# Optimization experiments

Measured on AMD Instinct MI355X. Metric: run time of the kernel, lower is better.

## Reference

```python
import jax, jax.numpy as jnp
import numpy as np

B = 64            # graphs in batch
N = 100_000       # total nodes
E = 600_000       # total edges of g == nodes of line graph lg
E2 = 1_500_000    # edges of line graph
H = 128           # hidden_dim
L = 3             # num_layers
MAXZ = 100

seg_sum = jax.ops.segment_sum


def setup_inputs() -> dict:
    key = jax.random.key(0)
    ks = jax.random.split(key, 20)
    s = 1.0 / np.sqrt(H)
    inp = {
        'z': jax.random.randint(ks[0], (N,), 0, MAXZ + 1),
        'd': jax.random.uniform(ks[1], (E, 1), dtype=jnp.float32),
        'src': jax.random.randint(ks[2], (E,), 0, N),
        'dst': jax.random.randint(ks[3], (E,), 0, N),
        'lsrc': jax.random.randint(ks[4], (E2,), 0, E),
        'ldst': jax.random.randint(ks[5], (E2,), 0, E),
        'node_graph': jnp.sort(jax.random.randint(ks[6], (N,), 0, B)),
        'edge_graph': jnp.sort(jax.random.randint(ks[7], (E,), 0, B)),
        'emb': jax.random.normal(ks[8], (MAXZ + 1, H), jnp.float32),
        'ep_w': jax.random.normal(ks[9], (1, H), jnp.float32) * s,
        'ep_b': jnp.zeros((H,), jnp.float32),
        'gW': jax.random.normal(ks[10], (L, H, H), jnp.float32) * s,
        'gb': jnp.zeros((L, H), jnp.float32),
        'lgW': jax.random.normal(ks[11], (L, H, H), jnp.float32) * s,
        'lgb': jnp.zeros((L, H), jnp.float32),
        'r1w': jax.random.normal(ks[12], (2 * H, H), jnp.float32) * s,
        'r1b': jnp.zeros((H,), jnp.float32),
        'r2w': jax.random.normal(ks[13], (H, 1), jnp.float32) * s,
        'r2b': jnp.zeros((1,), jnp.float32),
    }
    return inp


def _graph_conv(h, srcix, dstix, W, b, n_nodes):
    # DGL GraphConv, norm='both', aggregate-then-weight (in==out dims):
    # h' = D_in^{-1/2} * A^T * (D_out^{-1/2} * h) @ W + b, degrees clamped >= 1
    ones = jnp.ones(srcix.shape[0], h.dtype)
    deg_out = jnp.clip(seg_sum(ones, srcix, num_segments=n_nodes), 1.0)
    deg_in = jnp.clip(seg_sum(ones, dstix, num_segments=n_nodes), 1.0)
    m = h * (deg_out ** -0.5)[:, None]
    agg = seg_sum(m[srcix], dstix, num_segments=n_nodes)  # SpMM gather-scatter
    agg = agg * (deg_in ** -0.5)[:, None]
    return agg @ W + b


def _segment_mean(h, seg, n_seg):
    sums = seg_sum(h, seg, num_segments=n_seg)
    cnt = jnp.clip(seg_sum(jnp.ones(h.shape[0], h.dtype), seg, num_segments=n_seg), 1.0)
    return sums / cnt[:, None]


def reference(z, d, src, dst, lsrc, ldst, node_graph, edge_graph,
              emb, ep_w, ep_b, gW, gb, lgW, lgb, r1w, r1b, r2w, r2b):
    h = emb[z]                       # [N, H]
    e = d @ ep_w + ep_b              # [E, H]
    for i in range(L):
        h = jax.nn.relu(_graph_conv(h, src, dst, gW[i], gb[i], N))
    for i in range(L):
        e = jax.nn.relu(_graph_conv(e, lsrc, ldst, lgW[i], lgb[i], E))
    hg = _segment_mean(h, node_graph, B)   # [B, H]
    he = _segment_mean(e, edge_graph, B)   # [B, H]
    x = jnp.concatenate([hg, he], axis=-1)  # [B, 2H]
    y = jax.nn.silu(x @ r1w + r1b) @ r2w + r2b
    return y.reshape(-1)             # [B]
```

## Files before the change

kernel.cpp:

```cpp
#include <hip/hip_runtime.h>
#include <math.h>

#define H 128
typedef unsigned short u16;
typedef unsigned char u8;
typedef unsigned int u32;
typedef _Float16 f16;
typedef f16 f16x8 __attribute__((ext_vector_type(8)));
typedef float f32x4 __attribute__((ext_vector_type(4)));
typedef float f32x2 __attribute__((ext_vector_type(2)));

#if __has_builtin(__builtin_amdgcn_cvt_pk_fp8_f32)
#define HW8 1
#else
#define HW8 0
#endif

#define SSTRIDE 144

static inline int cdiv(long long a, long long b) { return (int)((a + b - 1) / b); }

struct F8 {
    static __device__ inline float dec(u8 v) {
        int e = (v >> 3) & 15, m = v & 7;
        float f = (e == 0) ? (float)m * 0.001953125f : ldexpf(1.f + 0.125f * (float)m, e - 7);
        return (v & 0x80) ? -f : f;
    }
    static __device__ inline u8 enc(float x) {
        u8 s = (u8)((__float_as_uint(x) >> 24) & 0x80);
        float ax = fabsf(x);
        if (!(ax < 448.f)) return s | 0x7E;
        if (ax < 0.015625f) {
            int m = (int)rintf(ax * 512.f);
            if (m >= 8) return s | 0x08;
            return s | (u8)m;
        }
        int e; float fr = frexpf(ax, &e);
        int E = e - 1;
        int m = (int)rintf(fr * 16.f - 8.f);
        if (m == 8) { m = 0; ++E; }
        if (E > 8) return s | 0x7E;
        return s | (u8)(((E + 7) << 3) | m);
    }
};

static __device__ inline u32 enc4(float x0, float x1, float x2, float x3) {
#if HW8
    u32 w = __builtin_amdgcn_cvt_pk_fp8_f32(x0, x1, 0, false);
    w = __builtin_amdgcn_cvt_pk_fp8_f32(x2, x3, w, true);
    return w;
#else
    union { u8 b[4]; u32 u; } p;
    p.b[0] = F8::enc(x0); p.b[1] = F8::enc(x1); p.b[2] = F8::enc(x2); p.b[3] = F8::enc(x3);
    return p.u;
#endif
}
static __device__ inline float4 dec4(u32 v) {
#if HW8
    f32x2 lo = __builtin_amdgcn_cvt_pk_f32_fp8(v, false);
    f32x2 hi = __builtin_amdgcn_cvt_pk_f32_fp8(v, true);
    return make_float4(lo.x, lo.y, hi.x, hi.y);
#else
    union { u32 u; u8 b[4]; } c; c.u = v;
    return make_float4(F8::dec(c.b[0]), F8::dec(c.b[1]), F8::dec(c.b[2]), F8::dec(c.b[3]));
#endif
}
static __device__ inline float dec1(u8 b) {
#if HW8
    return __builtin_amdgcn_cvt_f32_fp8((int)b, 0);
#else
    return F8::dec(b);
#endif
}

__global__ __launch_bounds__(256) void setup1_k(
    const float* __restrict__ gW, const float* __restrict__ lgW, f16* __restrict__ wt, int L, int nbPW,
    const int* __restrict__ src, const int* __restrict__ dst,
    const int* __restrict__ lsrc, const int* __restrict__ ldst,
    int* __restrict__ con, int* __restrict__ cin, int* __restrict__ coe, int* __restrict__ cie,
    int E, int E2, int nbHI,
    const int* __restrict__ node_graph, int N, const int* __restrict__ edge_graph,
    int B, int* __restrict__ cntn, int* __restrict__ cnte,
    const float* __restrict__ epw, const float* __restrict__ epb, float* __restrict__ uv) {
    int blk = blockIdx.x;
    if (blk < nbPW) {
        int mat = blk >> 6;
        int idx = (blk & 63) * 256 + threadIdx.x;
        int k = idx >> 7, n = idx & 127;
        const float* W = (mat < L) ? gW + (size_t)mat * H * H : lgW + (size_t)(mat - L) * H * H;
        wt[(size_t)mat * H * H + (size_t)n * H + k] = (f16)W[(size_t)k * H + n];
        return;
    }
    blk -= nbPW;
    if (blk < nbHI) {
        int i = blk * 256 + threadIdx.x;
        if (i < E) {
            atomicAdd(&con[src[i]], 1);
            atomicAdd(&cin[dst[i]], 1);
        } else if (i < E + E2) {
            int j = i - E;
            atomicAdd(&coe[lsrc[j]], 1);
            atomicAdd(&cie[ldst[j]], 1);
        }
        return;
    }
    blk -= nbHI;
    if (blk < 2) {
        const int* seg = blk ? edge_graph : node_graph;
        int n = blk ? E : N;
        int* cnt = blk ? cnte : cntn;
        __shared__ int bound[129];
        int b = threadIdx.x;
        if (b <= B) {
            int lo = 0, hi = n;
            while (lo < hi) {
                int mid = (lo + hi) >> 1;
                if (seg[mid] < b) lo = mid + 1; else hi = mid;
            }
            bound[b] = lo;
        }
        __syncthreads();
        if (b < B) cnt[b] = bound[b + 1] - bound[b];
        return;
    }
    {
        int n = threadIdx.x;
        if (n < H) {
            float su = 0.f, sv = 0.f;
            for (int k = 0; k < H; ++k) {
                float w = lgW[(size_t)k * H + n];
                su = fmaf(epw[k], w, su);
                sv = fmaf(epb[k], w, sv);
            }
            uv[n] = su;
            uv[n + H] = sv;
        }
    }
}

__global__ __launch_bounds__(256) void setup2_k(
    const int* __restrict__ con, const int* __restrict__ cin,
    const int* __restrict__ coe, const int* __restrict__ cie,
    float* __restrict__ ron, float* __restrict__ rin,
    float* __restrict__ roe, float* __restrict__ rie,
    const float* __restrict__ d, float2* __restrict__ pairE, int N, int E, int nbRS,
    int* __restrict__ offs_n, int nbN, int* __restrict__ offs_e, int* __restrict__ bsum) {
    int blk = blockIdx.x;
    if (blk < nbRS) {
        int i = blk * 256 + threadIdx.x;
        if (i < N) { int v = con[i]; ron[i] = rsqrtf((float)(v < 1 ? 1 : v)); }
        else if (i < 2 * N) { int n = i - N; int v = cin[n]; rin[n] = rsqrtf((float)(v < 1 ? 1 : v)); }
        else if (i < 2 * N + E) {
            int n = i - 2 * N; int v = coe[n];
            float r = rsqrtf((float)(v < 1 ? 1 : v));
            roe[n] = r;
            pairE[n] = make_float2(r * d[n], r);
        } else if (i < 2 * N + 2 * E) {
            int n = i - 2 * N - E; int v = cie[n]; rie[n] = rsqrtf((float)(v < 1 ? 1 : v));
        }
        return;
    }
    blk -= nbRS;
    {
        __shared__ int sh[256];
        const int* in; int* out; int n; int gid;
        if (blk < nbN) { in = cin; out = offs_n; n = N; gid = blk * 256 + threadIdx.x; }
        else { in = cie; out = offs_e; n = E; gid = (blk - nbN) * 256 + threadIdx.x; }
        int v = (gid < n) ? in[gid] : 0;
        sh[threadIdx.x] = v;
        __syncthreads();
        for (int off = 1; off < 256; off <<= 1) {
            int t = (threadIdx.x >= off) ? sh[threadIdx.x - off] : 0;
            __syncthreads();
            sh[threadIdx.x] += t;
            __syncthreads();
        }
        if (gid < n) out[gid] = sh[threadIdx.x] - v;
        if (threadIdx.x == 255) bsum[blk] = sh[255];
    }
}

__global__ __launch_bounds__(256) void scan_bsum2_k(int* __restrict__ bsum, int nbA, int nbB) {
    __shared__ int sh[256];
    __shared__ int carry;
#pragma unroll 1
    for (int part = 0; part < 2; ++part) {
        int base0 = part ? nbA : 0;
        int nb = part ? nbB : nbA;
        if (threadIdx.x == 0) carry = 0;
        __syncthreads();
        for (int base = 0; base < nb; base += 256) {
            int i = base + threadIdx.x;
            int v = (i < nb) ? bsum[base0 + i] : 0;
            sh[threadIdx.x] = v;
            __syncthreads();
            for (int off = 1; off < 256; off <<= 1) {
                int t = (threadIdx.x >= off) ? sh[threadIdx.x - off] : 0;
                __syncthreads();
                sh[threadIdx.x] += t;
                __syncthreads();
            }
            if (i < nb) bsum[base0 + i] = sh[threadIdx.x] - v + carry;
            __syncthreads();
            if (threadIdx.x == 0) carry += sh[255];
            __syncthreads();
        }
    }
}

__global__ __launch_bounds__(256) void setup3_k(
    int* __restrict__ offs_n, int* __restrict__ cur_n, int N, int nbN, int E,
    int* __restrict__ offs_e, int* __restrict__ cur_e, int E2, int nbE,
    const int* __restrict__ bsum,
    const int* __restrict__ z, const float* __restrict__ emb,
    const float* __restrict__ ron, u8* __restrict__ featN) {
    int blk = blockIdx.x;
    int nbSA = nbN + nbE;
    if (blk < nbSA) {
        int* offs; int* curp; int n; int gid; int nnz;
        if (blk < nbN) { offs = offs_n; curp = cur_n; n = N; gid = blk * 256 + threadIdx.x; nnz = E; }
        else { offs = offs_e; curp = cur_e; n = E; gid = (blk - nbN) * 256 + threadIdx.x; nnz = E2; }
        if (gid < n) {
            int v = offs[gid] + bsum[blk];
            offs[gid] = v;
            curp[gid] = v;
        }
        if (gid == 0) offs[n] = nnz;
        return;
    }
    blk -= nbSA;
    {
        int idx = blk * 256 + threadIdx.x;
        if (idx >= N * 32) return;
        int n = idx >> 5, c4 = (idx & 31) << 2;
        float sc = ron[n];
        const float4 v = *(const float4*)(emb + (size_t)z[n] * H + c4);
        *(u32*)(featN + (size_t)n * H + c4) = enc4(v.x * sc, v.y * sc, v.z * sc, v.w * sc);
    }
}

__global__ __launch_bounds__(256) void fill2_k(const int* __restrict__ src, const int* __restrict__ dst,
                                               const int* __restrict__ lsrc, const int* __restrict__ ldst,
                                               int* __restrict__ cur_n, int* __restrict__ cur_e,
                                               uint2* __restrict__ nbr_n, uint2* __restrict__ nbr_e,
                                               const float2* __restrict__ pairE, float2* __restrict__ pslot,
                                               int E, int E2) {
    int i = blockIdx.x * 256 + threadIdx.x;
    if (i < E) {
        int dd = dst[i];
        int p = atomicAdd(&cur_n[dd], 1);
        nbr_n[p] = make_uint2((u32)src[i], (u32)dd);
    } else if (i < E + E2) {
        int j = i - E;
        int ls = lsrc[j];
        int dd = ldst[j];
        int p = atomicAdd(&cur_e[dd], 1);
        nbr_e[p] = make_uint2((u32)ls, (u32)dd);
        pslot[p] = pairE[ls];
    }
}

__device__ __forceinline__ void gather_phase(
    const u8* __restrict__ Xin,
    const int* __restrict__ offs, const uint2* __restrict__ nbr2,
    const float* __restrict__ rs_in, int M,
    int row0, f16 (*As)[136], int wave, int lane) {
    const int rowbase = row0 + wave * 16;
    {
        uint2* zp = (uint2*)&As[wave * 16][0];
#pragma unroll
        for (int i = 0; i < 9; ++i) {
            int o = lane + i * 64;
            if (o < 544) zp[o] = make_uint2(0u, 0u);
        }
    }
    const int gl = lane >> 4;
    const int ln = lane & 15;
    const int rbase4 = rowbase + gl * 4;
    const int r_lo = min(rbase4, M);
    const int r_hi = min(rbase4 + 4, M);
    const int jbeg = offs[r_lo];
    const int jend = offs[r_hi];
    if (jbeg >= jend) return;
    const int mrow = M - 1;
    const float rsr0 = rs_in[min(rbase4 + 0, mrow)];
    const float rsr1 = rs_in[min(rbase4 + 1, mrow)];
    const float rsr2 = rs_in[min(rbase4 + 2, mrow)];
    const float rsr3 = rs_in[min(rbase4 + 3, mrow)];

    float a0 = 0.f, a1 = 0.f, a2 = 0.f, a3 = 0.f, a4 = 0.f, a5 = 0.f, a6 = 0.f, a7 = 0.f;
    int curdst = -1;

#define FLUSH_ROW()                                                              \
    do {                                                                         \
        const int dd_ = curdst - rbase4;                                         \
        const float ri_ = dd_ == 0 ? rsr0 : (dd_ == 1 ? rsr1 : (dd_ == 2 ? rsr2 : rsr3)); \
        f16x8 o_;                                                                \
        o_[0] = (f16)(a0 * ri_); o_[1] = (f16)(a1 * ri_);                        \
        o_[2] = (f16)(a2 * ri_); o_[3] = (f16)(a3 * ri_);                        \
        o_[4] = (f16)(a4 * ri_); o_[5] = (f16)(a5 * ri_);                        \
        o_[6] = (f16)(a6 * ri_); o_[7] = (f16)(a7 * ri_);                        \
        *(f16x8*)&As[curdst - row0][ln << 3] = o_;                               \
    } while (0)

    uint2 e[8];
#pragma unroll
    for (int k = 0; k < 8; ++k) e[k] = nbr2[min(jbeg + k, jend - 1)];
    int jc = jbeg;
    do {
        uint2 f[8];
#pragma unroll
        for (int k = 0; k < 8; ++k)
            f[k] = *(const uint2*)(Xin + ((size_t)e[k].x << 7) + (ln << 3));
        const int jn = jc + 8;
        uint2 en[8];
#pragma unroll
        for (int k = 0; k < 8; ++k) en[k] = nbr2[min(jn + k, jend - 1)];
#pragma unroll
        for (int k = 0; k < 8; ++k) {
            if (jc + k < jend) {
                const int dk = (int)e[k].y;
                if (dk != curdst) {
                    if (curdst >= 0) {
                        FLUSH_ROW();
                        a0 = a1 = a2 = a3 = a4 = a5 = a6 = a7 = 0.f;
                    }
                    curdst = dk;
                }
                float4 lo = dec4(f[k].x);
                float4 hi = dec4(f[k].y);
                a0 += lo.x; a1 += lo.y; a2 += lo.z; a3 += lo.w;
                a4 += hi.x; a5 += hi.y; a6 += hi.z; a7 += hi.w;
            }
        }
#pragma unroll
        for (int k = 0; k < 8; ++k) e[k] = en[k];
        jc = jn;
    } while (jc < jend);
    FLUSH_ROW();
#undef FLUSH_ROW
}

template <bool STORE>
__device__ __forceinline__ void conv_mfma_phase(
    u8* __restrict__ Xout, const f16* __restrict__ Wt, const float* __restrict__ bias,
    const float* __restrict__ scale_out, int M, int row0, f16 (*As)[136], int wave, int lane) {
    const int rowbase = row0 + wave * 16;
    if (rowbase >= M) return;
    const int l15 = lane & 15;
    const int quad = lane >> 4;

    f16x8 a[4];
#pragma unroll
    for (int kt = 0; kt < 4; ++kt)
        a[kt] = *(const f16x8*)&As[wave * 16 + l15][kt * 32 + quad * 8];

    float rsc[4];
#pragma unroll
    for (int r = 0; r < 4; ++r) {
        int gr = rowbase + quad * 4 + r;
        rsc[r] = (scale_out && gr < M) ? scale_out[gr] : 1.f;
    }

    u8* stage = (u8*)&As[wave * 16][0];

#pragma unroll
    for (int n0 = 0; n0 < 8; ++n0) {
        f32x4 acc = {0.f, 0.f, 0.f, 0.f};
        const f16* bp = Wt + (size_t)(n0 * 16 + l15) * H + quad * 8;
#pragma unroll
        for (int kt = 0; kt < 4; ++kt) {
            f16x8 b = *(const f16x8*)(bp + kt * 32);
            acc = __builtin_amdgcn_mfma_f32_16x16x32_f16(a[kt], b, acc, 0, 0, 0);
        }
        int col = n0 * 16 + l15;
        float bv = bias[col];
        float o[4];
#pragma unroll
        for (int r = 0; r < 4; ++r) o[r] = fmaxf(acc[r] + bv, 0.f) * rsc[r];
        u32 w = enc4(o[0], o[1], o[2], o[3]);
#pragma unroll
        for (int r = 0; r < 4; ++r) stage[(quad * 4 + r) * SSTRIDE + col] = (u8)(w >> (8 * r));
    }
    if (STORE) {
        const int lr = lane >> 2;
        const int lc = (lane & 3) * 32;
        int gr = rowbase + lr;
        if (gr < M) {
            uint4 v0 = *(const uint4*)&stage[lr * SSTRIDE + lc];
            uint4 v1 = *(const uint4*)&stage[lr * SSTRIDE + lc + 16];
            *(uint4*)(Xout + (size_t)gr * H + lc) = v0;
            *(uint4*)(Xout + (size_t)gr * H + lc + 16) = v1;
        }
    }
}

__device__ __forceinline__ void conv_mfma_pool_phase(
    const f16* __restrict__ Wt, const float* __restrict__ bias, int M, int row0,
    f16 (*As)[136], float (*pool)[128], int wave, int lane,
    const int* __restrict__ seg, float* __restrict__ outp, bool uni) {
    const int rowbase = row0 + wave * 16;
    if (rowbase >= M) return;
    const int l15 = lane & 15;
    const int quad = lane >> 4;

    f16x8 a[4];
#pragma unroll
    for (int kt = 0; kt < 4; ++kt)
        a[kt] = *(const f16x8*)&As[wave * 16 + l15][kt * 32 + quad * 8];

    const int gr0 = rowbase + quad * 4;
    const int remM = M - gr0;
    int g0 = -1, g1 = -1, g2 = -1, g3 = -1;
    if (!uni) {
        g0 = (0 < remM) ? seg[gr0 + 0] : -1;
        g1 = (1 < remM) ? seg[gr0 + 1] : -1;
        g2 = (2 < remM) ? seg[gr0 + 2] : -1;
        g3 = (3 < remM) ? seg[gr0 + 3] : -1;
    }

#pragma unroll
    for (int n0 = 0; n0 < 8; ++n0) {
        f32x4 acc = {0.f, 0.f, 0.f, 0.f};
        const f16* bp = Wt + (size_t)(n0 * 16 + l15) * H + quad * 8;
#pragma unroll
        for (int kt = 0; kt < 4; ++kt) {
            f16x8 b = *(const f16x8*)(bp + kt * 32);
            acc = __builtin_amdgcn_mfma_f32_16x16x32_f16(a[kt], b, acc, 0, 0, 0);
        }
        const int col = n0 * 16 + l15;
        const float bv = bias[col];
        const float o0 = (0 < remM) ? fmaxf(acc[0] + bv, 0.f) : 0.f;
        const float o1 = (1 < remM) ? fmaxf(acc[1] + bv, 0.f) : 0.f;
        const float o2 = (2 < remM) ? fmaxf(acc[2] + bv, 0.f) : 0.f;
        const float o3 = (3 < remM) ? fmaxf(acc[3] + bv, 0.f) : 0.f;
        if (uni) {
            float s = (o0 + o1) + (o2 + o3);
            s += __shfl_xor(s, 16);
            s += __shfl_xor(s, 32);
            if (quad == 0) pool[wave][col] = s;
        } else {
            float ac = o0; int gc = g0;
            if (g1 == gc) ac += o1; else { if (gc >= 0) atomicAdd(&outp[(size_t)gc * H + col], ac); gc = g1; ac = o1; }
            if (g2 == gc) ac += o2; else { if (gc >= 0) atomicAdd(&outp[(size_t)gc * H + col], ac); gc = g2; ac = o2; }
            if (g3 == gc) ac += o3; else { if (gc >= 0) atomicAdd(&outp[(size_t)gc * H + col], ac); gc = g3; ac = o3; }
            if (gc >= 0) atomicAdd(&outp[(size_t)gc * H + col], ac);
        }
    }
}

template <bool STORE>
__device__ __forceinline__ void conv_wave(
    const u8* __restrict__ Xin, u8* __restrict__ Xout,
    const int* __restrict__ offs, const uint2* __restrict__ nbr2,
    const float* __restrict__ rs_in, const f16* __restrict__ Wt,
    const float* __restrict__ bias, const float* __restrict__ scale_out, int M,
    int row0, f16 (*As)[136], int wave, int lane) {
    gather_phase(Xin, offs, nbr2, rs_in, M, row0, As, wave, lane);
    conv_mfma_phase<STORE>(Xout, Wt, bias, scale_out, M, row0, As, wave, lane);
}

__device__ __forceinline__ void conv_wave_l0e(
    u8* __restrict__ Xout, const int* __restrict__ offs,
    const float2* __restrict__ pslot, const float* __restrict__ rs_in,
    const float* __restrict__ uv, const float* __restrict__ bias,
    const float* __restrict__ scale_out, int E,
    int row0, int wave, int lane) {
    const int rowbase = row0 + wave * 16;
    const int r = lane >> 2;
    const int t = lane & 3;
    const int growu = rowbase + r;
    const int grow = min(growu, E - 1);
    const int jb = offs[grow];
    const int je = offs[grow + 1];
    float sd = 0.f, sw = 0.f;
    for (int j = jb + t; j < je; j += 4) {
        float2 p = pslot[j];
        sd += p.x; sw += p.y;
    }
    sd += __shfl_xor(sd, 1); sw += __shfl_xor(sw, 1);
    sd += __shfl_xor(sd, 2); sw += __shfl_xor(sw, 2);
    if (growu >= E) return;
    const float ri = rs_in[growu];
    const float so = scale_out[growu];
    sd *= ri; sw *= ri;
    const int c0 = t * 32;
    u32 wbuf[8];
#pragma unroll
    for (int c4 = 0; c4 < 8; ++c4) {
        const int c = c0 + c4 * 4;
        const float4 ua = *(const float4*)(uv + c);
        const float4 va = *(const float4*)(uv + H + c);
        const float4 ba = *(const float4*)(bias + c);
        const float o0 = fmaxf(fmaf(sd, ua.x, fmaf(sw, va.x, ba.x)), 0.f) * so;
        const float o1 = fmaxf(fmaf(sd, ua.y, fmaf(sw, va.y, ba.y)), 0.f) * so;
        const float o2 = fmaxf(fmaf(sd, ua.z, fmaf(sw, va.z, ba.z)), 0.f) * so;
        const float o3 = fmaxf(fmaf(sd, ua.w, fmaf(sw, va.w, ba.w)), 0.f) * so;
        wbuf[c4] = enc4(o0, o1, o2, o3);
    }
    *(uint4*)(Xout + (size_t)growu * H + c0) = *(uint4*)&wbuf[0];
    *(uint4*)(Xout + (size_t)growu * H + c0 + 16) = *(uint4*)&wbuf[4];
}

__global__ __launch_bounds__(256, 4) void conv2_k(
    const u8* __restrict__ XinN, u8* __restrict__ XoutN,
    const int* __restrict__ offs_n, const uint2* __restrict__ nbr_n,
    const float* __restrict__ rinN, const f16* __restrict__ WtN,
    const float* __restrict__ biasN, const float* __restrict__ scaleN, int N, int nbCN,
    const u8* __restrict__ XinE, u8* __restrict__ XoutE,
    const int* __restrict__ offs_e, const uint2* __restrict__ nbr_e,
    const float* __restrict__ rinE, const f16* __restrict__ WtE,
    const float* __restrict__ biasE, const float* __restrict__ scaleE, int E) {
    __shared__ f16 As[64][136];
    const int tid = threadIdx.x;
    const int wave = tid >> 6;
    const int lane = tid & 63;
    if ((int)blockIdx.x < nbCN) {
        conv_wave<true>(XinN, XoutN, offs_n, nbr_n, rinN, WtN, biasN, scaleN, N,
                        blockIdx.x * 64, As, wave, lane);
    } else {
        conv_wave<true>(XinE, XoutE, offs_e, nbr_e, rinE, WtE, biasE, scaleE, E,
                        (blockIdx.x - nbCN) * 64, As, wave, lane);
    }
}

__global__ __launch_bounds__(256, 4) void conv2_l0_k(
    const u8* __restrict__ XinN, u8* __restrict__ XoutN,
    const int* __restrict__ offs_n, const uint2* __restrict__ nbr_n,
    const float* __restrict__ rinN, const f16* __restrict__ WtN,
    const float* __restrict__ biasN, const float* __restrict__ scaleN, int N, int nbCN,
    u8* __restrict__ XoutE,
    const int* __restrict__ offs_e, const float2* __restrict__ pslot,
    const float* __restrict__ rinE, const float* __restrict__ uv,
    const float* __restrict__ biasE, const float* __restrict__ scaleE, int E) {
    __shared__ f16 As[64][136];
    const int tid = threadIdx.x;
    const int wave = tid >> 6;
    const int lane = tid & 63;
    if ((int)blockIdx.x < nbCN) {
        conv_wave<true>(XinN, XoutN, offs_n, nbr_n, rinN, WtN, biasN, scaleN, N,
                        blockIdx.x * 64, As, wave, lane);
    } else {
        conv_wave_l0e(XoutE, offs_e, pslot, rinE, uv, biasE, scaleE, E,
                      (blockIdx.x - nbCN) * 64, wave, lane);
    }
}

__global__ __launch_bounds__(256, 4) void conv2_last_k(
    const u8* __restrict__ XinN,
    const int* __restrict__ offs_n, const uint2* __restrict__ nbr_n,
    const float* __restrict__ rinN, const f16* __restrict__ WtN,
    const float* __restrict__ biasN, int N, int nbCN,
    const int* __restrict__ node_graph, float* __restrict__ hg,
    const u8* __restrict__ XinE,
    const int* __restrict__ offs_e, const uint2* __restrict__ nbr_e,
    const float* __restrict__ rinE, const f16* __restrict__ WtE,
    const float* __restrict__ biasE, int E,
    const int* __restrict__ edge_graph, float* __restrict__ he) {
    __shared__ f16 As[64][136];
    __shared__ float pool[4][128];
    const int tid = threadIdx.x;
    const int wave = tid >> 6;
    const int lane = tid & 63;
    const bool isN = (int)blockIdx.x < nbCN;
    const int row0 = (isN ? blockIdx.x : blockIdx.x - nbCN) * 64;
    const int M = isN ? N : E;
    const int* seg = isN ? node_graph : edge_graph;
    float* outp = isN ? hg : he;

    ((float*)pool)[tid] = 0.f;
    ((float*)pool)[tid + 256] = 0.f;
    const int gblk = seg[row0];
    const bool uni = (seg[min(row0 + 63, M - 1)] == gblk);
    __syncthreads();

    if (isN) {
        gather_phase(XinN, offs_n, nbr_n, rinN, N, row0, As, wave, lane);
        conv_mfma_pool_phase(WtN, biasN, N, row0, As, pool, wave, lane, seg, outp, uni);
    } else {
        gather_phase(XinE, offs_e, nbr_e, rinE, E, row0, As, wave, lane);
        conv_mfma_pool_phase(WtE, biasE, E, row0, As, pool, wave, lane, seg, outp, uni);
    }
    __syncthreads();
    if (uni && tid < 128) {
        float s = (pool[0][tid] + pool[1][tid]) + (pool[2][tid] + pool[3][tid]);
        atomicAdd(&outp[(size_t)gblk * H + tid], s);
    }
}

__global__ __launch_bounds__(128) void readout_k(const float* __restrict__ hg, const float* __restrict__ he,
                                                 const int* __restrict__ cn, const int* __restrict__ ce,
                                                 const float* __restrict__ r1w, const float* __restrict__ r1b,
                                                 const float* __restrict__ r2w, const float* __restrict__ r2b,
                                                 float* __restrict__ out) {
    const int b = blockIdx.x;
    const int j = threadIdx.x;
    const float invn = 1.f / fmaxf((float)cn[b], 1.f);
    const float inve = 1.f / fmaxf((float)ce[b], 1.f);
    float acc = r1b[j];
    for (int k = 0; k < H; ++k) acc = fmaf(hg[(size_t)b * H + k] * invn, r1w[(size_t)k * H + j], acc);
    for (int k = 0; k < H; ++k) acc = fmaf(he[(size_t)b * H + k] * inve, r1w[(size_t)(k + H) * H + j], acc);
    float s = acc / (1.f + expf(-acc));
    __shared__ float red[128];
    red[j] = s * r2w[j];
    __syncthreads();
    for (int off = 64; off > 0; off >>= 1) {
        if (j < off) red[j] += red[j + off];
        __syncthreads();
    }
    if (j == 0) out[b] = red[0] + r2b[0];
}

__global__ void report_k(float* out, int n, float val) {
    int i = blockIdx.x * 64 + threadIdx.x;
    if (i < n) out[i] = val;
}

extern "C" void kernel_launch(void* const* d_in, const int* in_sizes, int n_in,
                              void* d_out, int out_size, void* d_ws, size_t ws_size,
                              hipStream_t stream) {
    const int* z          = (const int*)d_in[0];
    const float* d        = (const float*)d_in[1];
    const int* src        = (const int*)d_in[2];
    const int* dst        = (const int*)d_in[3];
    const int* lsrc       = (const int*)d_in[4];
    const int* ldst       = (const int*)d_in[5];
    const int* node_graph = (const int*)d_in[6];
    const int* edge_graph = (const int*)d_in[7];
    const float* emb      = (const float*)d_in[8];
    const float* epw      = (const float*)d_in[9];
    const float* epb      = (const float*)d_in[10];
    const float* gW       = (const float*)d_in[11];
    const float* gb       = (const float*)d_in[12];
    const float* lgW      = (const float*)d_in[13];
    const float* lgb      = (const float*)d_in[14];
    const float* r1w      = (const float*)d_in[15];
    const float* r1b      = (const float*)d_in[16];
    const float* r2w      = (const float*)d_in[17];
    const float* r2b      = (const float*)d_in[18];

    const int N  = in_sizes[0];
    const int E  = in_sizes[2];
    const int E2 = in_sizes[4];
    const int B  = out_size;
    const int L  = 3;
    float* out = (float*)d_out;
    char* ws = (char*)d_ws;

    size_t off = 0;
    auto al = [&](size_t b) -> char* { char* q = ws + off; off += (b + 255) & ~(size_t)255; return q; };
    u8*  featEA = (u8*)al((size_t)E * H);
    u8*  featEB = (u8*)al((size_t)E * H);
    u8*  featNA = (u8*)al((size_t)N * H);
    u8*  featNB = (u8*)al((size_t)N * H);
    f16* wt    = (f16*)al((size_t)2 * L * H * H * 2);
    float* uv  = (float*)al((size_t)2 * H * 4);
    float* ron = (float*)al((size_t)N * 4);
    float* rin = (float*)al((size_t)N * 4);
    float* roe = (float*)al((size_t)E * 4);
    float* rie = (float*)al((size_t)E * 4);
    float2* pairE = (float2*)al((size_t)E * 8);
    size_t cntCount = (size_t)2 * N + 2 * E + 2 * B;
    size_t cntBytes = cntCount * 4;
    size_t poolsOff = (cntBytes + 255) & ~(size_t)255;
    char* zblock = al(poolsOff + (size_t)2 * B * H * 4);
    int* cnts = (int*)zblock;
    float* pools = (float*)(zblock + poolsOff);
    int* con = cnts; int* cin_ = con + N; int* coe = cin_ + N; int* cie = coe + E;
    int* cntn = cie + E; int* cnte = cntn + B;
    float* hg = pools;
    float* he = pools + (size_t)B * H;
    int* offs_n = (int*)al(((size_t)N + 1) * 4);
    int* cur_n  = (int*)al((size_t)N * 4);
    int* offs_e = (int*)al(((size_t)E + 1) * 4);
    int* cur_e  = (int*)al((size_t)E * 4);
    uint2* nbr_n = (uint2*)al((size_t)E * 8);
    uint2* nbr_e = (uint2*)al((size_t)E2 * 8);
    float2* pslot = (float2*)al((size_t)E2 * 8);
    int nbN = cdiv(N, 256), nbE = cdiv(E, 256);
    int* bsum   = (int*)al(((size_t)nbN + nbE + 2) * 4);

    if (off > ws_size) {
        report_k<<<cdiv(B, 64), 64, 0, stream>>>(out, B, (float)(ws_size >> 20));
        return;
    }

    hipMemsetAsync(zblock, 0, poolsOff + (size_t)2 * B * H * 4, stream);

    const int nbPW = 2 * L * 64;
    const int nbHI = cdiv((long long)E + E2, 256);
    setup1_k<<<nbPW + nbHI + 3, 256, 0, stream>>>(gW, lgW, wt, L, nbPW,
                                                  src, dst, lsrc, ldst, con, cin_, coe, cie,
                                                  E, E2, nbHI, node_graph, N, edge_graph, B, cntn, cnte,
                                                  epw, epb, uv);

    const int nbRS = cdiv((long long)2 * N + 2 * E, 256);
    setup2_k<<<nbRS + nbN + nbE, 256, 0, stream>>>(con, cin_, coe, cie, ron, rin, roe, rie,
                                                   d, pairE, N, E, nbRS, offs_n, nbN, offs_e, bsum);
    scan_bsum2_k<<<1, 256, 0, stream>>>(bsum, nbN, nbE);

    const int nbIN = cdiv((long long)N * 32, 256);
    setup3_k<<<nbN + nbE + nbIN, 256, 0, stream>>>(offs_n, cur_n, N, nbN, E,
                                                   offs_e, cur_e, E2, nbE, bsum, z, emb, ron, featNA);

    fill2_k<<<cdiv((long long)E + E2, 256), 256, 0, stream>>>(src, dst, lsrc, ldst, cur_n, cur_e,
                                                              nbr_n, nbr_e, pairE, pslot, E, E2);

    const int nbCN = cdiv(N, 64), nbCE = cdiv(E, 64);

    conv2_l0_k<<<nbCN + nbCE, 256, 0, stream>>>(
        featNA, featNB, offs_n, nbr_n, rin, wt, gb, ron, N, nbCN,
        featEB, offs_e, pslot, rie, uv, lgb, roe, E);

    conv2_k<<<nbCN + nbCE, 256, 0, stream>>>(
        featNB, featNA, offs_n, nbr_n, rin, wt + (size_t)1 * H * H, gb + (size_t)1 * H, ron, N, nbCN,
        featEB, featEA, offs_e, nbr_e, rie, wt + (size_t)(L + 1) * H * H, lgb + (size_t)1 * H, roe, E);

    conv2_last_k<<<nbCN + nbCE, 256, 0, stream>>>(
        featNA, offs_n, nbr_n, rin, wt + (size_t)2 * H * H, gb + (size_t)2 * H, N, nbCN, node_graph, hg,
        featEA, offs_e, nbr_e, rie, wt + (size_t)(L + 2) * H * H, lgb + (size_t)2 * H, E, edge_graph, he);

    readout_k<<<B, 128, 0, stream>>>(hg, he, cntn, cnte, r1w, r1b, r2w, r2b, out);
}
```

Before: 1.001 ms.

## Double-buffer gather loads and swizzle block IDs across XCDs

The gather loop now uses two stages of software pipelining. Feature rows for the next group of 8 neighbours are issued before the current group is accumulated, and neighbour indices are prefetched two groups ahead, which hides more gather latency. The fused conv kernels also remap blockIdx so consecutive logical blocks land on the same XCD, aiming for better L2 locality of the destination-sorted gathers. The cost is higher register pressure from the extra uint2 buffers, which under launch_bounds(256,4) may cause spills or lower occupancy.

```diff
diff --git a/kernel.cpp b/kernel.cpp
--- a/kernel.cpp
+++ b/kernel.cpp
@@ -19,6 +19,13 @@
 #define SSTRIDE 144
 
 static inline int cdiv(long long a, long long b) { return (int)((a + b - 1) / b); }
+
+__device__ __forceinline__ int xcd_swz(int orig, int nwg) {
+    int q = nwg >> 3, r = nwg & 7;
+    int xcd = orig & 7;
+    int base = (xcd < r) ? xcd * (q + 1) : r * (q + 1) + (xcd - r) * q;
+    return base + (orig >> 3);
+}
 
 struct F8 {
     static __device__ inline float dec(u8 v) {
@@ -303,23 +310,29 @@
         *(f16x8*)&As[curdst - row0][ln << 3] = o_;                               \
     } while (0)
 
-    uint2 e[8];
-#pragma unroll
-    for (int k = 0; k < 8; ++k) e[k] = nbr2[min(jbeg + k, jend - 1)];
+    uint2 eA[8], eB[8], fA[8], fB[8], eN[8];
+#pragma unroll
+    for (int k = 0; k < 8; ++k) eA[k] = nbr2[min(jbeg + k, jend - 1)];
+#pragma unroll
+    for (int k = 0; k < 8; ++k) eB[k] = nbr2[min(jbeg + 8 + k, jend - 1)];
+#pragma unroll
+    for (int k = 0; k < 8; ++k)
+        fA[k] = *(const uint2*)(Xin + ((size_t)eA[k].x << 7) + (ln << 3));
     int jc = jbeg;
-    do {
-        uint2 f[8];
-#pragma unroll
-        for (int k = 0; k < 8; ++k)
-            f[k] = *(const uint2*)(Xin + ((size_t)e[k].x << 7) + (ln << 3));
+    while (true) {
         const int jn = jc + 8;
-        uint2 en[8];
-#pragma unroll
-        for (int k = 0; k < 8; ++k) en[k] = nbr2[min(jn + k, jend - 1)];
+        const bool more = jn < jend;
+        if (more) {
+#pragma unroll
+            for (int k = 0; k < 8; ++k)
+                fB[k] = *(const uint2*)(Xin + ((size_t)eB[k].x << 7) + (ln << 3));
+#pragma unroll
+            for (int k = 0; k < 8; ++k) eN[k] = nbr2[min(jn + 8 + k, jend - 1)];
+        }
 #pragma unroll
         for (int k = 0; k < 8; ++k) {
             if (jc + k < jend) {
-                const int dk = (int)e[k].y;
+                const int dk = (int)eA[k].y;
                 if (dk != curdst) {
                     if (curdst >= 0) {
                         FLUSH_ROW();
@@ -327,16 +340,17 @@
                     }
                     curdst = dk;
                 }
-                float4 lo = dec4(f[k].x);
-                float4 hi = dec4(f[k].y);
+                float4 lo = dec4(fA[k].x);
+                float4 hi = dec4(fA[k].y);
                 a0 += lo.x; a1 += lo.y; a2 += lo.z; a3 += lo.w;
                 a4 += hi.x; a5 += hi.y; a6 += hi.z; a7 += hi.w;
             }
         }
-#pragma unroll
-        for (int k = 0; k < 8; ++k) e[k] = en[k];
+        if (!more) break;
+#pragma unroll
+        for (int k = 0; k < 8; ++k) { eA[k] = eB[k]; eB[k] = eN[k]; fA[k] = fB[k]; }
         jc = jn;
-    } while (jc < jend);
+    }
     FLUSH_ROW();
 #undef FLUSH_ROW
 }
@@ -515,12 +529,13 @@
     const int tid = threadIdx.x;
     const int wave = tid >> 6;
     const int lane = tid & 63;
-    if ((int)blockIdx.x < nbCN) {
+    const int bid = xcd_swz((int)blockIdx.x, (int)gridDim.x);
+    if (bid < nbCN) {
         conv_wave<true>(XinN, XoutN, offs_n, nbr_n, rinN, WtN, biasN, scaleN, N,
-                        blockIdx.x * 64, As, wave, lane);
+                        bid * 64, As, wave, lane);
     } else {
         conv_wave<true>(XinE, XoutE, offs_e, nbr_e, rinE, WtE, biasE, scaleE, E,
-                        (blockIdx.x - nbCN) * 64, As, wave, lane);
+                        (bid - nbCN) * 64, As, wave, lane);
     }
 }
 
@@ -537,12 +552,13 @@
     const int tid = threadIdx.x;
     const int wave = tid >> 6;
     const int lane = tid & 63;
-    if ((int)blockIdx.x < nbCN) {
+    const int bid = xcd_swz((int)blockIdx.x, (int)gridDim.x);
+    if (bid < nbCN) {
         conv_wave<true>(XinN, XoutN, offs_n, nbr_n, rinN, WtN, biasN, scaleN, N,
-                        blockIdx.x * 64, As, wave, lane);
+                        bid * 64, As, wave, lane);
     } else {
         conv_wave_l0e(XoutE, offs_e, pslot, rinE, uv, biasE, scaleE, E,
-                      (blockIdx.x - nbCN) * 64, wave, lane);
+                      (bid - nbCN) * 64, wave, lane);
     }
 }
 
@@ -562,8 +578,9 @@
     const int tid = threadIdx.x;
     const int wave = tid >> 6;
     const int lane = tid & 63;
-    const bool isN = (int)blockIdx.x < nbCN;
-    const int row0 = (isN ? blockIdx.x : blockIdx.x - nbCN) * 64;
+    const int bid = xcd_swz((int)blockIdx.x, (int)gridDim.x);
+    const bool isN = bid < nbCN;
+    const int row0 = (isN ? bid : bid - nbCN) * 64;
     const int M = isN ? N : E;
     const int* seg = isN ? node_graph : edge_graph;
     float* outp = isN ? hg : he;
```

After: 1.180 ms. 17.9% more time.
